# Performance work log

Measured on AMD Instinct MI355X. Metric: run time of the kernel, lower is better.

Reference implementation:

```python
import jax, jax.numpy as jnp
import numpy as np

HIDDEN = 1024
N_EXPERTS = 8
TOP_K = 2
INTER = 1408
NORM_TOPK = False


def setup_inputs() -> dict:
    key = jax.random.key(0)
    ks = jax.random.split(key, 5)
    B, S = 4, 2048
    scale_h = 1.0 / np.sqrt(HIDDEN)
    scale_i = 1.0 / np.sqrt(INTER)
    return {
        "hidden_states": jax.random.normal(ks[0], (B, S, HIDDEN), dtype=jnp.float32),
        "gate_w": jax.random.normal(ks[1], (N_EXPERTS, HIDDEN), dtype=jnp.float32) * scale_h,  # router
        "w_gate": jax.random.normal(ks[2], (N_EXPERTS, HIDDEN, INTER), dtype=jnp.float32) * scale_h,
        "w_up": jax.random.normal(ks[3], (N_EXPERTS, HIDDEN, INTER), dtype=jnp.float32) * scale_h,
        "w_down": jax.random.normal(ks[4], (N_EXPERTS, INTER, HIDDEN), dtype=jnp.float32) * scale_i,
    }


def reference(hidden_states, gate_w, w_gate, w_up, w_down):
    B, S, H = hidden_states.shape
    x = hidden_states.reshape(-1, H)                     # [T, H]
    T = x.shape[0]

    router_logits = x @ gate_w.T                          # [T, E]
    probs = jax.nn.softmax(router_logits.astype(jnp.float32), axis=-1)
    topk_w, topk_idx = jax.lax.top_k(probs, TOP_K)        # [T, K]
    if NORM_TOPK:
        topk_w = topk_w / jnp.sum(topk_w, axis=-1, keepdims=True)
    topk_w = topk_w.astype(x.dtype)

    # Scatter top-k weights into dense [T, E] combine weights (0 for unselected).
    weights = jnp.zeros((T, N_EXPERTS), dtype=x.dtype)
    weights = weights.at[jnp.arange(T)[:, None], topk_idx].set(topk_w)

    # Dense grouped SwiGLU over all experts; combine masks out unrouted pairs.
    g = jnp.einsum('th,ehi->eti', x, w_gate)              # [E, T, I]
    u = jnp.einsum('th,ehi->eti', x, w_up)                # [E, T, I]
    y = jnp.einsum('eti,eih->eth', jax.nn.silu(g) * u, w_down)  # [E, T, H]
    final = jnp.einsum('eth,te->th', y, weights)          # [T, H]

    return final.reshape(B, S, H), router_logits
```

## Files before the change

kernel.cpp:

```cpp
#include <hip/hip_runtime.h>
#include <hip/hip_bf16.h>
#include <math.h>

#define T_TOK 8192
#define HID   1024
#define NE    8
#define TOPKN 2
#define INTER 1408
#define NROWS (T_TOK*TOPKN)
#define MAXWL 144
#define RBLK  256

typedef __attribute__((ext_vector_type(8))) __bf16 bf16x8;
typedef __attribute__((ext_vector_type(4))) float f32x4;
typedef __attribute__((ext_vector_type(4))) unsigned int u32x4;

__device__ __forceinline__ unsigned short f2bf(float f) {
    unsigned int u = __builtin_bit_cast(unsigned int, f);
    unsigned int lsb = (u >> 16) & 1u;
    u += 0x7fffu + lsb;
    return (unsigned short)(u >> 16);
}

__device__ __forceinline__ void gl2lds16(const void* g, void* l) {
    __builtin_amdgcn_global_load_lds(
        (const __attribute__((address_space(1))) unsigned int*)g,
        (__attribute__((address_space(3))) unsigned int*)l, 16, 0, 0);
}

__global__ __launch_bounds__(256) void moe_router(
    const float* __restrict__ x, const float* __restrict__ gate_w,
    unsigned short* __restrict__ xb, float* __restrict__ logits_out,
    int* __restrict__ topk_idx, float* __restrict__ topk_w,
    int* __restrict__ hist_g)
{
    __shared__ int lh[NE];
    int tid = threadIdx.x, wave = tid >> 6, lane = tid & 63;
    if (tid < NE) lh[tid] = 0;
    __syncthreads();

#pragma unroll 1
    for (int i = 0; i < 8; i++) {
        int t = blockIdx.x * 32 + wave * 8 + i;
        const float4* xr = (const float4*)(x + (size_t)t * HID);
        float acc[NE];
#pragma unroll
        for (int e = 0; e < NE; e++) acc[e] = 0.f;
#pragma unroll
        for (int j = 0; j < 4; j++) {
            float4 xv = xr[j * 64 + lane];
            ushort4 pk;
            pk.x = f2bf(xv.x); pk.y = f2bf(xv.y);
            pk.z = f2bf(xv.z); pk.w = f2bf(xv.w);
            *(ushort4*)(xb + (size_t)t * HID + j * 256 + lane * 4) = pk;
#pragma unroll
            for (int e = 0; e < NE; e++) {
                float4 gv = *(const float4*)(gate_w + e * HID + j * 256 + lane * 4);
                acc[e] += xv.x * gv.x + xv.y * gv.y + xv.z * gv.z + xv.w * gv.w;
            }
        }
#pragma unroll
        for (int e = 0; e < NE; e++) {
            float v = acc[e];
#pragma unroll
            for (int off = 32; off; off >>= 1) v += __shfl_xor(v, off, 64);
            acc[e] = v;
        }
        if (lane == 0) {
            float m = acc[0];
#pragma unroll
            for (int e = 1; e < NE; e++) m = fmaxf(m, acc[e]);
            float p[NE]; float s = 0.f;
#pragma unroll
            for (int e = 0; e < NE; e++) { p[e] = expf(acc[e] - m); s += p[e]; }
            float inv = 1.f / s;
#pragma unroll
            for (int e = 0; e < NE; e++) logits_out[(size_t)t * NE + e] = acc[e];
            int i0 = 0;
#pragma unroll
            for (int e = 1; e < NE; e++) if (p[e] > p[i0]) i0 = e;
            int i1 = (i0 == 0) ? 1 : 0;
#pragma unroll
            for (int e = 0; e < NE; e++) if (e != i0 && p[e] > p[i1]) i1 = e;
            topk_idx[2 * t]     = i0; topk_w[2 * t]     = p[i0] * inv;
            topk_idx[2 * t + 1] = i1; topk_w[2 * t + 1] = p[i1] * inv;
            atomicAdd(&lh[i0], 1);
            atomicAdd(&lh[i1], 1);
        }
    }
    __syncthreads();
    if (tid < NE) hist_g[blockIdx.x * NE + tid] = lh[tid];
}

__global__ __launch_bounds__(256) void moe_scan(
    const int* __restrict__ hist_g, int* __restrict__ offsets,
    int* __restrict__ block_base, int* __restrict__ wl, int* __restrict__ n_wl)
{
    __shared__ int h[RBLK * NE];
    __shared__ int cnt[NE], offs[NE];
    int tid = threadIdx.x;
    for (int i = tid; i < RBLK * NE; i += 256) h[i] = hist_g[i];
    __syncthreads();
    {
        int e = tid >> 5, g = tid & 31;
        int s = 0;
        for (int b = g; b < RBLK; b += 32) s += h[b * NE + e];
#pragma unroll
        for (int off2 = 16; off2; off2 >>= 1) s += __shfl_xor(s, off2, 32);
        if (g == 0) cnt[e] = s;
    }
    __syncthreads();
    if (tid == 0) {
        int s = 0;
        for (int e = 0; e < NE; e++) { offs[e] = s; offsets[e] = s; s += cnt[e]; }
        offsets[NE] = s;
        int n = 0;
        for (int e = 0; e < NE; e++)
            for (int r0 = 0; r0 < cnt[e]; r0 += 128)
                wl[n++] = (e << 24) | r0;
        *n_wl = n;
    }
    __syncthreads();
    if (tid < NE) {
        int run = offs[tid];
        for (int b = 0; b < RBLK; b++) {
            block_base[b * NE + tid] = run;
            run += h[b * NE + tid];
        }
    }
}

__global__ __launch_bounds__(64) void moe_scatter(
    const int* __restrict__ topk_idx, const float* __restrict__ topk_w,
    const int* __restrict__ block_base, int* __restrict__ row_token,
    float* __restrict__ row_w, int* __restrict__ tok_rows)
{
    __shared__ int base[NE];
    int tid = threadIdx.x;
    if (tid < NE) base[tid] = block_base[blockIdx.x * NE + tid];
    __syncthreads();
    int idx = blockIdx.x * 64 + tid;
    int e = topk_idx[idx];
    int pos = atomicAdd(&base[e], 1);
    row_token[pos] = idx >> 1;
    row_w[pos] = topk_w[idx];
    tok_rows[idx] = pos;
}

__global__ __launch_bounds__(256) void moe_transpose_cast(
    const float* __restrict__ in, unsigned short* __restrict__ out,
    int R_, int C_)
{
    __shared__ float tile[64][65];
    int e = blockIdx.z;
    const float* ine = in + (size_t)e * R_ * C_;
    unsigned short* oute = out + (size_t)e * R_ * C_;
    int c0 = blockIdx.x * 64, r0 = blockIdx.y * 64;
    int tid = threadIdx.x;
    int lr = tid >> 4;
    int lc = tid & 15;
#pragma unroll
    for (int j = 0; j < 4; j++) {
        int r = lr + j * 16;
        float4 v = *(const float4*)(ine + (size_t)(r0 + r) * C_ + c0 + lc * 4);
        tile[r][lc * 4 + 0] = v.x; tile[r][lc * 4 + 1] = v.y;
        tile[r][lc * 4 + 2] = v.z; tile[r][lc * 4 + 3] = v.w;
    }
    __syncthreads();
#pragma unroll
    for (int j = 0; j < 4; j++) {
        int c = (tid >> 4) + j * 16;
        int r = (tid & 15) * 4;
        ushort4 pk;
        pk.x = f2bf(tile[r + 0][c]);
        pk.y = f2bf(tile[r + 1][c]);
        pk.z = f2bf(tile[r + 2][c]);
        pk.w = f2bf(tile[r + 3][c]);
        *(ushort4*)(oute + (size_t)(c0 + c) * R_ + r0 + r) = pk;
    }
}

__global__ __launch_bounds__(256) void moe_gemm1(
    const unsigned short* __restrict__ xb,
    const unsigned short* __restrict__ wg_t,
    const unsigned short* __restrict__ wu_t,
    const int* __restrict__ offsets, const int* __restrict__ row_token,
    const int* __restrict__ wl, const int* __restrict__ n_wl,
    unsigned short* __restrict__ h_buf)
{
    if ((int)blockIdx.y >= *n_wl) return;
    int wle = wl[blockIdx.y];
    int e = wle >> 24, row0 = wle & 0xffffff;
    int off = offsets[e], cnt = offsets[e + 1] - off;
    int i0 = blockIdx.x * 64;

    __shared__ __align__(16) unsigned short As[2][128 * 64];
    __shared__ __align__(16) unsigned short Bg[2][64 * 64];
    __shared__ __align__(16) unsigned short Bu[2][64 * 64];

    int tid = threadIdx.x, wave = tid >> 6, lane = tid & 63;
    int wm = wave & 1, wn = wave >> 1;
    int l16 = lane & 15, quad = lane >> 4;
    int r_ = lane >> 3, c_ = lane & 7;
    int sw = l16 & 7;

    const unsigned short* asrc[4];
#pragma unroll
    for (int it = 0; it < 4; it++) {
        int rloc = it * 32 + wave * 8 + r_;
        int rg = row0 + rloc;
        int tok = row_token[off + ((rg < cnt) ? rg : 0)];
        asrc[it] = xb + (size_t)tok * HID + (c_ ^ (rloc & 7)) * 8;
    }
    const unsigned short* bgsrc[2];
    const unsigned short* busrc[2];
#pragma unroll
    for (int it = 0; it < 2; it++) {
        int rloc = it * 32 + wave * 8 + r_;
        size_t boff = (size_t)e * INTER * HID + (size_t)(i0 + rloc) * HID + (c_ ^ (rloc & 7)) * 8;
        bgsrc[it] = wg_t + boff;
        busrc[it] = wu_t + boff;
    }

    f32x4 accg[4][2], accu[4][2];
#pragma unroll
    for (int mi = 0; mi < 4; mi++)
#pragma unroll
        for (int ni = 0; ni < 2; ni++) {
            accg[mi][ni] = {0.f, 0.f, 0.f, 0.f};
            accu[mi][ni] = {0.f, 0.f, 0.f, 0.f};
        }

    auto stage = [&](unsigned short* asb, unsigned short* bgb, unsigned short* bub, int k0) {
#pragma unroll
        for (int it = 0; it < 4; it++)
            gl2lds16(asrc[it] + k0, asb + (it * 32 + wave * 8) * 64);
#pragma unroll
        for (int it = 0; it < 2; it++) {
            gl2lds16(bgsrc[it] + k0, bgb + (it * 32 + wave * 8) * 64);
            gl2lds16(busrc[it] + k0, bub + (it * 32 + wave * 8) * 64);
        }
    };
    auto compute = [&](const unsigned short* asb, const unsigned short* bgb,
                       const unsigned short* bub) {
#pragma unroll
        for (int kk8 = 0; kk8 < 8; kk8 += 4) {
            int q = kk8 + quad;
            int qs = (q ^ sw) * 8;
            bf16x8 a[4], bg[2], bu[2];
#pragma unroll
            for (int mi = 0; mi < 4; mi++)
                a[mi] = *(const bf16x8*)&asb[(wm * 64 + mi * 16 + l16) * 64 + qs];
#pragma unroll
            for (int ni = 0; ni < 2; ni++) {
                bg[ni] = *(const bf16x8*)&bgb[(wn * 32 + ni * 16 + l16) * 64 + qs];
                bu[ni] = *(const bf16x8*)&bub[(wn * 32 + ni * 16 + l16) * 64 + qs];
            }
#pragma unroll
            for (int mi = 0; mi < 4; mi++)
#pragma unroll
                for (int ni = 0; ni < 2; ni++) {
                    accg[mi][ni] = __builtin_amdgcn_mfma_f32_16x16x32_bf16(a[mi], bg[ni], accg[mi][ni], 0, 0, 0);
                    accu[mi][ni] = __builtin_amdgcn_mfma_f32_16x16x32_bf16(a[mi], bu[ni], accu[mi][ni], 0, 0, 0);
                }
        }
    };

    stage(As[0], Bg[0], Bu[0], 0);
    __syncthreads();
#pragma unroll 1
    for (int t = 0; t < 16; t += 2) {
        stage(As[1], Bg[1], Bu[1], (t + 1) * 64);
        compute(As[0], Bg[0], Bu[0]);
        __syncthreads();
        if (t + 2 < 16) stage(As[0], Bg[0], Bu[0], (t + 2) * 64);
        compute(As[1], Bg[1], Bu[1]);
        __syncthreads();
    }

#pragma unroll
    for (int mi = 0; mi < 4; mi++)
#pragma unroll
        for (int ni = 0; ni < 2; ni++)
#pragma unroll
            for (int r = 0; r < 4; r++) {
                int ml = wm * 64 + mi * 16 + quad * 4 + r;
                int row = row0 + ml;
                if (row < cnt) {
                    float g = accg[mi][ni][r], u = accu[mi][ni][r];
                    float hv = (g / (1.f + expf(-g))) * u;
                    h_buf[(size_t)(off + row) * INTER + i0 + wn * 32 + ni * 16 + l16] = f2bf(hv);
                }
            }
}

__global__ __launch_bounds__(256) void moe_gemm2(
    const unsigned short* __restrict__ h_buf,
    const unsigned short* __restrict__ wd_t,
    const int* __restrict__ offsets, const float* __restrict__ row_w,
    const int* __restrict__ wl, const int* __restrict__ n_wl,
    unsigned short* __restrict__ y_buf)
{
    if ((int)blockIdx.y >= *n_wl) return;
    int wle = wl[blockIdx.y];
    int e = wle >> 24, row0 = wle & 0xffffff;
    int off = offsets[e], cnt = offsets[e + 1] - off;
    int h0 = blockIdx.x * 128;

    __shared__ __align__(16) unsigned short As[2][128 * 64];
    __shared__ __align__(16) unsigned short Bs[2][128 * 64];

    int tid = threadIdx.x, wave = tid >> 6, lane = tid & 63;
    int wm = wave & 1, wn = wave >> 1;
    int l16 = lane & 15, quad = lane >> 4;
    int r_ = lane >> 3, c_ = lane & 7;
    int sw = l16 & 7;

    const unsigned short* asrc[4];
    const unsigned short* bsrc[4];
#pragma unroll
    for (int it = 0; it < 4; it++) {
        int rloc = it * 32 + wave * 8 + r_;
        int rg = row0 + rloc;
        asrc[it] = h_buf + (size_t)(off + ((rg < cnt) ? rg : 0)) * INTER + (c_ ^ (rloc & 7)) * 8;
        bsrc[it] = wd_t + (size_t)e * HID * INTER + (size_t)(h0 + rloc) * INTER + (c_ ^ (rloc & 7)) * 8;
    }

    f32x4 acc[4][4];
#pragma unroll
    for (int mi = 0; mi < 4; mi++)
#pragma unroll
        for (int ni = 0; ni < 4; ni++) acc[mi][ni] = {0.f, 0.f, 0.f, 0.f};

    auto stage = [&](unsigned short* asb, unsigned short* bsb, int k0) {
#pragma unroll
        for (int it = 0; it < 4; it++) {
            gl2lds16(asrc[it] + k0, asb + (it * 32 + wave * 8) * 64);
            gl2lds16(bsrc[it] + k0, bsb + (it * 32 + wave * 8) * 64);
        }
    };
    auto compute = [&](const unsigned short* asb, const unsigned short* bsb) {
#pragma unroll
        for (int kk8 = 0; kk8 < 8; kk8 += 4) {
            int q = kk8 + quad;
            int qs = (q ^ sw) * 8;
            bf16x8 a[4], b[4];
#pragma unroll
            for (int mi = 0; mi < 4; mi++)
                a[mi] = *(const bf16x8*)&asb[(wm * 64 + mi * 16 + l16) * 64 + qs];
#pragma unroll
            for (int ni = 0; ni < 4; ni++)
                b[ni] = *(const bf16x8*)&bsb[(wn * 64 + ni * 16 + l16) * 64 + qs];
#pragma unroll
            for (int mi = 0; mi < 4; mi++)
#pragma unroll
                for (int ni = 0; ni < 4; ni++)
                    acc[mi][ni] = __builtin_amdgcn_mfma_f32_16x16x32_bf16(a[mi], b[ni], acc[mi][ni], 0, 0, 0);
        }
    };

    stage(As[0], Bs[0], 0);
    __syncthreads();
#pragma unroll 1
    for (int t = 0; t < 22; t += 2) {
        stage(As[1], Bs[1], (t + 1) * 64);
        compute(As[0], Bs[0]);
        __syncthreads();
        if (t + 2 < 22) stage(As[0], Bs[0], (t + 2) * 64);
        compute(As[1], Bs[1]);
        __syncthreads();
    }

#pragma unroll
    for (int mi = 0; mi < 4; mi++)
#pragma unroll
        for (int ni = 0; ni < 4; ni++)
#pragma unroll
            for (int r = 0; r < 4; r++) {
                int ml = wm * 64 + mi * 16 + quad * 4 + r;
                int row = row0 + ml;
                if (row < cnt) {
                    float w = row_w[off + row];
                    y_buf[(size_t)(off + row) * HID + h0 + wn * 64 + ni * 16 + l16] =
                        f2bf(acc[mi][ni][r] * w);
                }
            }
}

__global__ __launch_bounds__(256) void moe_combine(
    const unsigned short* __restrict__ y_buf, const int* __restrict__ tok_rows,
    float* __restrict__ out)
{
    int gid = blockIdx.x * 256 + threadIdx.x;
    int t = gid >> 7;
    int c = gid & 127;
    u32x4 a = *(const u32x4*)(y_buf + (size_t)tok_rows[2 * t]     * HID + c * 8);
    u32x4 b = *(const u32x4*)(y_buf + (size_t)tok_rows[2 * t + 1] * HID + c * 8);
    float res[8];
#pragma unroll
    for (int j = 0; j < 4; j++) {
        unsigned int wa = a[j], wb = b[j];
        res[2 * j]     = __builtin_bit_cast(float, wa << 16)
                       + __builtin_bit_cast(float, wb << 16);
        res[2 * j + 1] = __builtin_bit_cast(float, wa & 0xffff0000u)
                       + __builtin_bit_cast(float, wb & 0xffff0000u);
    }
    float* o = out + (size_t)t * HID + c * 8;
    *(float4*)(o)     = make_float4(res[0], res[1], res[2], res[3]);
    *(float4*)(o + 4) = make_float4(res[4], res[5], res[6], res[7]);
}

extern "C" void kernel_launch(void* const* d_in, const int* in_sizes, int n_in,
                              void* d_out, int out_size, void* d_ws, size_t ws_size,
                              hipStream_t stream)
{
    const float* x      = (const float*)d_in[0];
    const float* gate_w = (const float*)d_in[1];
    const float* w_gate = (const float*)d_in[2];
    const float* w_up   = (const float*)d_in[3];
    const float* w_down = (const float*)d_in[4];
    float* out = (float*)d_out;
    float* logits_out = out + (size_t)T_TOK * HID;

    char* ws = (char*)d_ws;
    int*   offsets    = (int*)(ws + 0);
    int*   n_wl       = (int*)(ws + 64);
    int*   wl         = (int*)(ws + 128);
    int*   hist_g     = (int*)(ws + 1024);
    int*   block_base = (int*)(ws + 1024 + 8192);
    int*   topk_idx   = (int*)(ws + 32768);
    float* topk_w     = (float*)(ws + 32768 + 65536);
    int*   row_token  = (int*)(ws + 32768 + 2 * 65536);
    float* row_w      = (float*)(ws + 32768 + 3 * 65536);
    int*   tok_rows   = (int*)(ws + 32768 + 4 * 65536);
    size_t o = 32768 + 5 * (size_t)65536 + 32768;
    unsigned short* xb   = (unsigned short*)(ws + o); o += (size_t)T_TOK * HID * 2;
    unsigned short* wg_t = (unsigned short*)(ws + o); o += (size_t)NE * INTER * HID * 2;
    unsigned short* wu_t = (unsigned short*)(ws + o); o += (size_t)NE * INTER * HID * 2;
    unsigned short* wd_t = (unsigned short*)(ws + o); o += (size_t)NE * HID * INTER * 2;
    unsigned short* h_buf = (unsigned short*)(ws + o); o += (size_t)NROWS * INTER * 2;
    unsigned short* y_buf = (unsigned short*)(ws + o); o += (size_t)NROWS * HID * 2;

    moe_router<<<RBLK, 256, 0, stream>>>(x, gate_w, xb, logits_out,
                                         topk_idx, topk_w, hist_g);
    moe_scan<<<1, 256, 0, stream>>>(hist_g, offsets, block_base, wl, n_wl);
    moe_scatter<<<RBLK, 64, 0, stream>>>(topk_idx, topk_w, block_base,
                                         row_token, row_w, tok_rows);
    moe_transpose_cast<<<dim3(INTER / 64, HID / 64, NE), 256, 0, stream>>>(w_gate, wg_t, HID, INTER);
    moe_transpose_cast<<<dim3(INTER / 64, HID / 64, NE), 256, 0, stream>>>(w_up,   wu_t, HID, INTER);
    moe_transpose_cast<<<dim3(HID / 64, INTER / 64, NE), 256, 0, stream>>>(w_down, wd_t, INTER, HID);

    moe_gemm1<<<dim3(INTER / 64, MAXWL), 256, 0, stream>>>(
        xb, wg_t, wu_t, offsets, row_token, wl, n_wl, h_buf);
    moe_gemm2<<<dim3(HID / 128, MAXWL), 256, 0, stream>>>(
        h_buf, wd_t, offsets, row_w, wl, n_wl, y_buf);
    moe_combine<<<(T_TOK * HID / 8) / 256, 256, 0, stream>>>(y_buf, tok_rows, out);
}
```

Measured before the change: 468.0 us.

## Enlarge gemm1 tile to 256x128 with interleaved gate/up B and split-phase pipeline

Rewrites the gate/up GEMM to use 512-thread blocks that each compute a 256-row by 128-column output tile. Gate and up weight rows are interleaved in one shared B buffer, so each A fragment feeds both projections. The K loop is split into four phases, each with a partial vmcnt wait, a barrier and MFMA sections raised by setprio. Next-stage loads are issued between phases to overlap memory with compute. The scan kernel now also builds a 256-row work list. The aim is more data reuse per loaded byte and less global traffic, at the cost of 128KB of LDS per block and higher register pressure.

```diff
diff --git a/kernel.cpp b/kernel.cpp
--- a/kernel.cpp
+++ b/kernel.cpp
@@ -9,6 +9,7 @@
 #define INTER 1408
 #define NROWS (T_TOK*TOPKN)
 #define MAXWL 144
+#define MAXWL256 72
 #define RBLK  256
 
 typedef __attribute__((ext_vector_type(8))) __bf16 bf16x8;
@@ -94,7 +95,8 @@
 
 __global__ __launch_bounds__(256) void moe_scan(
     const int* __restrict__ hist_g, int* __restrict__ offsets,
-    int* __restrict__ block_base, int* __restrict__ wl, int* __restrict__ n_wl)
+    int* __restrict__ block_base, int* __restrict__ wl, int* __restrict__ n_wl,
+    int* __restrict__ wl256, int* __restrict__ n_wl256)
 {
     __shared__ int h[RBLK * NE];
     __shared__ int cnt[NE], offs[NE];
@@ -119,6 +121,11 @@
             for (int r0 = 0; r0 < cnt[e]; r0 += 128)
                 wl[n++] = (e << 24) | r0;
         *n_wl = n;
+        int n2 = 0;
+        for (int e = 0; e < NE; e++)
+            for (int r0 = 0; r0 < cnt[e]; r0 += 256)
+                wl256[n2++] = (e << 24) | r0;
+        *n_wl256 = n2;
     }
     __syncthreads();
     if (tid < NE) {
@@ -180,7 +187,7 @@
     }
 }
 
-__global__ __launch_bounds__(256) void moe_gemm1(
+__global__ __launch_bounds__(512, 2) void moe_gemm1(
     const unsigned short* __restrict__ xb,
     const unsigned short* __restrict__ wg_t,
     const unsigned short* __restrict__ wu_t,
@@ -192,104 +199,130 @@
     int wle = wl[blockIdx.y];
     int e = wle >> 24, row0 = wle & 0xffffff;
     int off = offsets[e], cnt = offsets[e + 1] - off;
-    int i0 = blockIdx.x * 64;
-
-    __shared__ __align__(16) unsigned short As[2][128 * 64];
-    __shared__ __align__(16) unsigned short Bg[2][64 * 64];
-    __shared__ __align__(16) unsigned short Bu[2][64 * 64];
+    int i0 = blockIdx.x * 128;
+
+    __shared__ __align__(16) unsigned short As[32768];
+    __shared__ __align__(16) unsigned short Bs[32768];
 
     int tid = threadIdx.x, wave = tid >> 6, lane = tid & 63;
     int wm = wave & 1, wn = wave >> 1;
     int l16 = lane & 15, quad = lane >> 4;
-    int r_ = lane >> 3, c_ = lane & 7;
-    int sw = l16 & 7;
-
-    const unsigned short* asrc[4];
-#pragma unroll
-    for (int it = 0; it < 4; it++) {
-        int rloc = it * 32 + wave * 8 + r_;
-        int rg = row0 + rloc;
-        int tok = row_token[off + ((rg < cnt) ? rg : 0)];
-        asrc[it] = xb + (size_t)tok * HID + (c_ ^ (rloc & 7)) * 8;
-    }
-    const unsigned short* bgsrc[2];
-    const unsigned short* busrc[2];
-#pragma unroll
-    for (int it = 0; it < 2; it++) {
-        int rloc = it * 32 + wave * 8 + r_;
-        size_t boff = (size_t)e * INTER * HID + (size_t)(i0 + rloc) * HID + (c_ ^ (rloc & 7)) * 8;
-        bgsrc[it] = wg_t + boff;
-        busrc[it] = wu_t + boff;
-    }
-
-    f32x4 accg[4][2], accu[4][2];
-#pragma unroll
-    for (int mi = 0; mi < 4; mi++)
-#pragma unroll
-        for (int ni = 0; ni < 2; ni++) {
-            accg[mi][ni] = {0.f, 0.f, 0.f, 0.f};
-            accu[mi][ni] = {0.f, 0.f, 0.f, 0.f};
-        }
-
-    auto stage = [&](unsigned short* asb, unsigned short* bgb, unsigned short* bub, int k0) {
-#pragma unroll
-        for (int it = 0; it < 4; it++)
-            gl2lds16(asrc[it] + k0, asb + (it * 32 + wave * 8) * 64);
-#pragma unroll
-        for (int it = 0; it < 2; it++) {
-            gl2lds16(bgsrc[it] + k0, bgb + (it * 32 + wave * 8) * 64);
-            gl2lds16(busrc[it] + k0, bub + (it * 32 + wave * 8) * 64);
-        }
-    };
-    auto compute = [&](const unsigned short* asb, const unsigned short* bgb,
-                       const unsigned short* bub) {
-#pragma unroll
-        for (int kk8 = 0; kk8 < 8; kk8 += 4) {
-            int q = kk8 + quad;
-            int qs = (q ^ sw) * 8;
-            bf16x8 a[4], bg[2], bu[2];
-#pragma unroll
-            for (int mi = 0; mi < 4; mi++)
-                a[mi] = *(const bf16x8*)&asb[(wm * 64 + mi * 16 + l16) * 64 + qs];
-#pragma unroll
-            for (int ni = 0; ni < 2; ni++) {
-                bg[ni] = *(const bf16x8*)&bgb[(wn * 32 + ni * 16 + l16) * 64 + qs];
-                bu[ni] = *(const bf16x8*)&bub[(wn * 32 + ni * 16 + l16) * 64 + qs];
-            }
-#pragma unroll
-            for (int mi = 0; mi < 4; mi++)
-#pragma unroll
-                for (int ni = 0; ni < 2; ni++) {
-                    accg[mi][ni] = __builtin_amdgcn_mfma_f32_16x16x32_bf16(a[mi], bg[ni], accg[mi][ni], 0, 0, 0);
-                    accu[mi][ni] = __builtin_amdgcn_mfma_f32_16x16x32_bf16(a[mi], bu[ni], accu[mi][ni], 0, 0, 0);
-                }
-        }
-    };
-
-    stage(As[0], Bg[0], Bu[0], 0);
-    __syncthreads();
+    int fsw = (l16 >> 1) & 3;
+
+    int kswz = ((lane & 3) ^ ((lane >> 3) & 3)) * 8;
+    int r0s = wave * 32 + (lane >> 2);
+    int r1s = r0s + 16;
+
+    int gA0 = row0 + r0s, gA1 = row0 + r1s;
+    int tok0 = row_token[off + ((gA0 < cnt) ? gA0 : 0)];
+    int tok1 = row_token[off + ((gA1 < cnt) ? gA1 : 0)];
+    const unsigned short* aptr0 = xb + (size_t)tok0 * HID + kswz;
+    const unsigned short* aptr1 = xb + (size_t)tok1 * HID + kswz;
+
+    int ic0 = i0 + (r0s >> 6) * 32 + (r0s & 31);
+    int ic1 = i0 + (r1s >> 6) * 32 + (r1s & 31);
+    const unsigned short* bptr0 =
+        (((r0s >> 5) & 1) ? wu_t : wg_t) + (size_t)e * INTER * HID + (size_t)ic0 * HID + kswz;
+    const unsigned short* bptr1 =
+        (((r1s >> 5) & 1) ? wu_t : wg_t) + (size_t)e * INTER * HID + (size_t)ic1 * HID + kswz;
+
+    f32x4 acc[8][4];
+#pragma unroll
+    for (int mi = 0; mi < 8; mi++)
+#pragma unroll
+        for (int ni = 0; ni < 4; ni++) acc[mi][ni] = {0.f, 0.f, 0.f, 0.f};
+
+    {
+        unsigned short* dA = &As[wave * 1024];
+        unsigned short* dB = &Bs[wave * 1024];
+        gl2lds16(aptr0, dA);            gl2lds16(aptr1, dA + 512);
+        gl2lds16(bptr0, dB);            gl2lds16(bptr1, dB + 512);
+        gl2lds16(aptr0 + 32, dA + 8192); gl2lds16(aptr1 + 32, dA + 8192 + 512);
+        gl2lds16(bptr0 + 32, dB + 8192); gl2lds16(bptr1 + 32, dB + 8192 + 512);
+    }
+    __syncthreads();
+
 #pragma unroll 1
-    for (int t = 0; t < 16; t += 2) {
-        stage(As[1], Bg[1], Bu[1], (t + 1) * 64);
-        compute(As[0], Bg[0], Bu[0]);
-        __syncthreads();
-        if (t + 2 < 16) stage(As[0], Bg[0], Bu[0], (t + 2) * 64);
-        compute(As[1], Bg[1], Bu[1]);
-        __syncthreads();
-    }
-
-#pragma unroll
-    for (int mi = 0; mi < 4; mi++)
-#pragma unroll
-        for (int ni = 0; ni < 2; ni++)
+    for (int kt = 0; kt < 16; kt++) {
+        const unsigned short* Ac = &As[(kt & 1) << 14];
+        const unsigned short* Bc = &Bs[(kt & 1) << 14];
+        unsigned short* An = &As[(((kt + 1) & 1) << 14) + wave * 1024];
+        unsigned short* Bn = &Bs[(((kt + 1) & 1) << 14) + wave * 1024];
+        int kb = (kt + 1) * 64;
+        bool more = kt < 15;
+        bf16x8 a[8], b0, b1;
+
+        asm volatile("s_waitcnt vmcnt(4)" ::: "memory");
+        __builtin_amdgcn_s_barrier();
+#pragma unroll
+        for (int mi = 0; mi < 8; mi++)
+            a[mi] = *(const bf16x8*)&Ac[(wm * 128 + mi * 16 + l16) * 32 + (quad ^ fsw) * 8];
+        b0 = *(const bf16x8*)&Bc[(wn * 64 + l16) * 32 + (quad ^ fsw) * 8];
+        b1 = *(const bf16x8*)&Bc[(wn * 64 + 16 + l16) * 32 + (quad ^ fsw) * 8];
+        if (more) { gl2lds16(aptr0 + kb, An); gl2lds16(aptr1 + kb, An + 512); }
+        __builtin_amdgcn_s_setprio(1);
+#pragma unroll
+        for (int mi = 0; mi < 8; mi++) {
+            acc[mi][0] = __builtin_amdgcn_mfma_f32_16x16x32_bf16(a[mi], b0, acc[mi][0], 0, 0, 0);
+            acc[mi][1] = __builtin_amdgcn_mfma_f32_16x16x32_bf16(a[mi], b1, acc[mi][1], 0, 0, 0);
+        }
+        __builtin_amdgcn_s_setprio(0);
+
+        asm volatile("s_waitcnt vmcnt(4)" ::: "memory");
+        __builtin_amdgcn_s_barrier();
+        b0 = *(const bf16x8*)&Bc[(wn * 64 + 32 + l16) * 32 + (quad ^ fsw) * 8];
+        b1 = *(const bf16x8*)&Bc[(wn * 64 + 48 + l16) * 32 + (quad ^ fsw) * 8];
+        if (more) { gl2lds16(bptr0 + kb, Bn); gl2lds16(bptr1 + kb, Bn + 512); }
+        __builtin_amdgcn_s_setprio(1);
+#pragma unroll
+        for (int mi = 0; mi < 8; mi++) {
+            acc[mi][2] = __builtin_amdgcn_mfma_f32_16x16x32_bf16(a[mi], b0, acc[mi][2], 0, 0, 0);
+            acc[mi][3] = __builtin_amdgcn_mfma_f32_16x16x32_bf16(a[mi], b1, acc[mi][3], 0, 0, 0);
+        }
+        __builtin_amdgcn_s_setprio(0);
+
+        asm volatile("s_waitcnt vmcnt(4)" ::: "memory");
+        __builtin_amdgcn_s_barrier();
+#pragma unroll
+        for (int mi = 0; mi < 8; mi++)
+            a[mi] = *(const bf16x8*)&Ac[8192 + (wm * 128 + mi * 16 + l16) * 32 + (quad ^ fsw) * 8];
+        b0 = *(const bf16x8*)&Bc[8192 + (wn * 64 + l16) * 32 + (quad ^ fsw) * 8];
+        b1 = *(const bf16x8*)&Bc[8192 + (wn * 64 + 16 + l16) * 32 + (quad ^ fsw) * 8];
+        if (more) { gl2lds16(aptr0 + kb + 32, An + 8192); gl2lds16(aptr1 + kb + 32, An + 8192 + 512); }
+        __builtin_amdgcn_s_setprio(1);
+#pragma unroll
+        for (int mi = 0; mi < 8; mi++) {
+            acc[mi][0] = __builtin_amdgcn_mfma_f32_16x16x32_bf16(a[mi], b0, acc[mi][0], 0, 0, 0);
+            acc[mi][1] = __builtin_amdgcn_mfma_f32_16x16x32_bf16(a[mi], b1, acc[mi][1], 0, 0, 0);
+        }
+        __builtin_amdgcn_s_setprio(0);
+
+        asm volatile("s_waitcnt vmcnt(4)" ::: "memory");
+        __builtin_amdgcn_s_barrier();
+        b0 = *(const bf16x8*)&Bc[8192 + (wn * 64 + 32 + l16) * 32 + (quad ^ fsw) * 8];
+        b1 = *(const bf16x8*)&Bc[8192 + (wn * 64 + 48 + l16) * 32 + (quad ^ fsw) * 8];
+        if (more) { gl2lds16(bptr0 + kb + 32, Bn + 8192); gl2lds16(bptr1 + kb + 32, Bn + 8192 + 512); }
+        __builtin_amdgcn_s_setprio(1);
+#pragma unroll
+        for (int mi = 0; mi < 8; mi++) {
+            acc[mi][2] = __builtin_amdgcn_mfma_f32_16x16x32_bf16(a[mi], b0, acc[mi][2], 0, 0, 0);
+            acc[mi][3] = __builtin_amdgcn_mfma_f32_16x16x32_bf16(a[mi], b1, acc[mi][3], 0, 0, 0);
+        }
+        __builtin_amdgcn_s_setprio(0);
+    }
+
+#pragma unroll
+    for (int mi = 0; mi < 8; mi++)
+#pragma unroll
+        for (int np = 0; np < 2; np++)
 #pragma unroll
             for (int r = 0; r < 4; r++) {
-                int ml = wm * 64 + mi * 16 + quad * 4 + r;
+                int ml = wm * 128 + mi * 16 + quad * 4 + r;
                 int row = row0 + ml;
                 if (row < cnt) {
-                    float g = accg[mi][ni][r], u = accu[mi][ni][r];
+                    float g = acc[mi][np][r], u = acc[mi][np + 2][r];
                     float hv = (g / (1.f + expf(-g))) * u;
-                    h_buf[(size_t)(off + row) * INTER + i0 + wn * 32 + ni * 16 + l16] = f2bf(hv);
+                    h_buf[(size_t)(off + row) * INTER + i0 + wn * 32 + np * 16 + l16] = f2bf(hv);
                 }
             }
 }
@@ -425,7 +458,9 @@
     char* ws = (char*)d_ws;
     int*   offsets    = (int*)(ws + 0);
     int*   n_wl       = (int*)(ws + 64);
+    int*   n_wl256    = (int*)(ws + 68);
     int*   wl         = (int*)(ws + 128);
+    int*   wl256      = (int*)(ws + 704);
     int*   hist_g     = (int*)(ws + 1024);
     int*   block_base = (int*)(ws + 1024 + 8192);
     int*   topk_idx   = (int*)(ws + 32768);
@@ -443,15 +478,16 @@
 
     moe_router<<<RBLK, 256, 0, stream>>>(x, gate_w, xb, logits_out,
                                          topk_idx, topk_w, hist_g);
-    moe_scan<<<1, 256, 0, stream>>>(hist_g, offsets, block_base, wl, n_wl);
+    moe_scan<<<1, 256, 0, stream>>>(hist_g, offsets, block_base, wl, n_wl,
+                                    wl256, n_wl256);
     moe_scatter<<<RBLK, 64, 0, stream>>>(topk_idx, topk_w, block_base,
                                          row_token, row_w, tok_rows);
     moe_transpose_cast<<<dim3(INTER / 64, HID / 64, NE), 256, 0, stream>>>(w_gate, wg_t, HID, INTER);
     moe_transpose_cast<<<dim3(INTER / 64, HID / 64, NE), 256, 0, stream>>>(w_up,   wu_t, HID, INTER);
     moe_transpose_cast<<<dim3(HID / 64, INTER / 64, NE), 256, 0, stream>>>(w_down, wd_t, INTER, HID);
 
-    moe_gemm1<<<dim3(INTER / 64, MAXWL), 256, 0, stream>>>(
-        xb, wg_t, wu_t, offsets, row_token, wl, n_wl, h_buf);
+    moe_gemm1<<<dim3(INTER / 128, MAXWL256), 512, 0, stream>>>(
+        xb, wg_t, wu_t, offsets, row_token, wl256, n_wl256, h_buf);
     moe_gemm2<<<dim3(HID / 128, MAXWL), 256, 0, stream>>>(
         h_buf, wd_t, offsets, row_w, wl, n_wl, y_buf);
     moe_combine<<<(T_TOK * HID / 8) / 256, 256, 0, stream>>>(y_buf, tok_rows, out);
```

New measurement: 459.4 us. About the same (-1.9%).
